# Performance work log

Hardware: AMD Instinct MI355X
Metric: run time of the kernel (lower is better)

Reference implementation:

```python
import jax, jax.numpy as jnp
import numpy as np

B, M = 1024, 200000
D_IN, DIM, D_OUT = 256, 128, 10
T = 1.0
EPS = 1e-7


def setup_inputs() -> dict:
    key = jax.random.key(0)
    k1, k2, k3, k4, k5 = jax.random.split(key, 5)
    x = jax.random.normal(k1, (B, D_IN), dtype=jnp.float32)
    y = jax.random.randint(k2, (B,), 0, D_OUT)
    candidate_x = jax.random.normal(k3, (M, D_IN), dtype=jnp.float32)
    candidate_y = jax.random.randint(k4, (M,), 0, D_OUT)
    W_enc = jax.random.normal(k5, (DIM, D_IN), dtype=jnp.float32) * (1.0 / np.sqrt(D_IN))
    b_enc = jnp.zeros((DIM,), dtype=jnp.float32)
    return {"x": x, "y": y, "candidate_x": candidate_x, "candidate_y": candidate_y,
            "W_enc": W_enc, "b_enc": b_enc, "is_train": 0}


def reference(x, y, candidate_x, candidate_y, W_enc, b_enc, is_train):
    # eval path (is_train == 0): no candidate subsampling, no diagonal masking
    h = x @ W_enc.T + b_enc            # [B, DIM]
    hc = candidate_x @ W_enc.T + b_enc  # [M, DIM]
    # pairwise L2 distance (cdist, p=2)
    sq = jnp.sum(h * h, axis=-1, keepdims=True) + jnp.sum(hc * hc, axis=-1)[None, :] \
         - 2.0 * (h @ hc.T)            # [B, M]
    dist = jnp.sqrt(jnp.maximum(sq, 0.0)) / T
    p = jax.nn.softmax(-dist, axis=-1)  # [B, M]
    y1h = jax.nn.one_hot(candidate_y, D_OUT, dtype=h.dtype)  # [M, D_OUT]
    logits = p @ y1h                    # [B, D_OUT]
    return jnp.log(logits + EPS)
```

## Files before the change

### kernel.cpp

```cpp
#include <hip/hip_runtime.h>
#include <hip/hip_bf16.h>
#include <math.h>

#define B_N   1024
#define M_N   200000
#define DIN   256
#define DIMN  128
#define DOUT  10
#define EPS_F 1e-7f
#define M_PAD 200064
#define NBY   1563
#define CTILES 8

typedef __bf16 bf16_t;
typedef __bf16 bf16x8 __attribute__((ext_vector_type(8)));
typedef float  f32x4  __attribute__((ext_vector_type(4)));


__global__ void cvt_w_kernel(const float* __restrict__ W, bf16_t* __restrict__ Wb){
    int i = blockIdx.x*256 + threadIdx.x;
    if (i < DIMN*DIN) Wb[i] = (bf16_t)W[i];
}

__global__ void hist_kernel(const int* __restrict__ cy, int* __restrict__ hist){
    __shared__ int h[DOUT];
    if (threadIdx.x < DOUT) h[threadIdx.x] = 0;
    __syncthreads();
    for (int i = blockIdx.x*blockDim.x + threadIdx.x; i < M_N; i += gridDim.x*blockDim.x)
        atomicAdd(&h[cy[i]], 1);
    __syncthreads();
    if (threadIdx.x < DOUT) atomicAdd(&hist[threadIdx.x*16], h[threadIdx.x]);
}

__global__ void prefix_kernel(const int* __restrict__ hist, int* __restrict__ cs){
    if (threadIdx.x == 0 && blockIdx.x == 0){
        int acc = 0;
        for (int c = 0; c < DOUT; ++c){ cs[c] = acc; acc += hist[c*16]; }
        cs[DOUT] = acc;
    }
}


__global__ __launch_bounds__(256) void encode_kernel(
    const float* __restrict__ src, const bf16_t* __restrict__ Wb,
    bf16_t* __restrict__ out, float* __restrict__ onorm, int N,
    const int* __restrict__ ycls, int* __restrict__ counters,
    const int* __restrict__ cs)
{
    __shared__ bf16_t As[128][136];
    __shared__ int   posL[128];
    __shared__ float nbuf[128][2];
    __shared__ int   cntL[DOUT], baseL[DOUT];
    const int tid = threadIdx.x;
    const int r0  = blockIdx.x*128;

    int myc = -1, myrank = 0;
    if (ycls != nullptr){
        if (tid < DOUT) cntL[tid] = 0;
        __syncthreads();
        if (tid < 128 && r0 + tid < N){
            myc = ycls[r0 + tid];
            myrank = atomicAdd(&cntL[myc], 1);
        }
        __syncthreads();
        if (tid < DOUT && cntL[tid] > 0)
            baseL[tid] = atomicAdd(&counters[tid*16], cntL[tid]);
        __syncthreads();
    }
    if (tid < 128)
        posL[tid] = (myc >= 0) ? (cs[myc] + baseL[myc] + myrank) : (r0 + tid);

    const int lane = tid & 63, wid = tid >> 6;
    const int wr = wid >> 1, wc = wid & 1;
    const int l15 = lane & 15, quad = lane >> 4;
    const int cbase = wc*64;

    f32x4 acc[4][4] = {};
    #pragma unroll
    for (int kh = 0; kh < 2; ++kh){
        __syncthreads();
        #pragma unroll
        for (int i = 0; i < 8; ++i){
            int idx = i*256 + tid;
            int row = idx >> 4;
            int col = (idx & 15)*8;
            int rr  = r0 + row; if (rr > N-1) rr = N-1;
            const float4* p4 = (const float4*)(src + (size_t)rr*DIN + kh*128 + col);
            float4 f0 = p4[0], f1 = p4[1];
            bf16x8 v;
            v[0]=(bf16_t)f0.x; v[1]=(bf16_t)f0.y; v[2]=(bf16_t)f0.z; v[3]=(bf16_t)f0.w;
            v[4]=(bf16_t)f1.x; v[5]=(bf16_t)f1.y; v[6]=(bf16_t)f1.z; v[7]=(bf16_t)f1.w;
            *(bf16x8*)&As[row][col] = v;
        }
        __syncthreads();
        #pragma unroll
        for (int ks = 0; ks < 4; ++ks){
            const int k  = ks*32 + quad*8;
            const int kg = kh*128 + k;
            bf16x8 a[4], b[4];
            #pragma unroll
            for (int rt = 0; rt < 4; ++rt)
                a[rt] = *(const bf16x8*)&As[wr*64 + rt*16 + l15][k];
            #pragma unroll
            for (int ct = 0; ct < 4; ++ct)
                b[ct] = *(const bf16x8*)(Wb + (size_t)(cbase + ct*16 + l15)*DIN + kg);
            #pragma unroll
            for (int rt = 0; rt < 4; ++rt)
                #pragma unroll
                for (int ct = 0; ct < 4; ++ct)
                    acc[rt][ct] = __builtin_amdgcn_mfma_f32_16x16x32_bf16(a[rt], b[ct], acc[rt][ct], 0, 0, 0);
        }
    }

    float np[4][4];
    #pragma unroll
    for (int rt = 0; rt < 4; ++rt)
        #pragma unroll
        for (int r = 0; r < 4; ++r){
            float s = 0.f;
            #pragma unroll
            for (int ct = 0; ct < 4; ++ct){ float v = acc[rt][ct][r]; s += v*v; }
            np[rt][r] = s;
        }
    #pragma unroll
    for (int m = 1; m < 16; m <<= 1)
        #pragma unroll
        for (int rt = 0; rt < 4; ++rt)
            #pragma unroll
            for (int r = 0; r < 4; ++r)
                np[rt][r] += __shfl_xor(np[rt][r], m, 64);
    if (l15 == 0){
        #pragma unroll
        for (int rt = 0; rt < 4; ++rt)
            #pragma unroll
            for (int r = 0; r < 4; ++r)
                nbuf[wr*64 + rt*16 + quad*4 + r][wc] = np[rt][r];
    }

    #pragma unroll
    for (int rt = 0; rt < 4; ++rt){
        #pragma unroll
        for (int r = 0; r < 4; ++r){
            int rl = wr*64 + rt*16 + quad*4 + r;
            if (r0 + rl < N){
                size_t rowp = (size_t)posL[rl]*DIMN;
                #pragma unroll
                for (int ct = 0; ct < 4; ++ct)
                    out[rowp + cbase + ct*16 + l15] = (bf16_t)acc[rt][ct][r];
            }
        }
    }
    __syncthreads();
    if (tid < 128){
        int rs = r0 + tid;
        if (rs < N) onorm[posL[tid]] = nbuf[tid][0] + nbuf[tid][1];
    }
}


__device__ __forceinline__ void bfly16(float (&s)[4][4]){
    #pragma unroll
    for (int m = 1; m < 16; m <<= 1)
        #pragma unroll
        for (int rt = 0; rt < 4; ++rt)
            #pragma unroll
            for (int r = 0; r < 4; ++r)
                s[rt][r] += __shfl_xor(s[rt][r], m, 64);
}

__device__ __forceinline__ void flushC(float (&s)[4][4], int c, int rbase,
                                       int quad, int l15, float* __restrict__ accG){
    bfly16(s);
    if (l15 == 0){
        #pragma unroll
        for (int rt = 0; rt < 4; ++rt)
            #pragma unroll
            for (int r = 0; r < 4; ++r)
                atomicAdd(&accG[(size_t)(rbase + rt*16 + quad*4 + r)*16 + c], s[rt][r]);
    }
}

__global__ __launch_bounds__(256, 2) void fused_kernel(
    const bf16_t* __restrict__ hb, const bf16_t* __restrict__ hcb,
    const float* __restrict__ hn, const float* __restrict__ hcn,
    const int* __restrict__ csg, float* __restrict__ accG)
{
    __shared__ bf16_t Bs[128][136];
    const int tid = threadIdx.x;
    const int lane = tid & 63, wid = tid >> 6;
    const int wr = wid >> 1, wc = wid & 1;
    const int l15 = lane & 15, quad = lane >> 4;
    const int rbase = blockIdx.x*128 + wr*64;

    bf16x8 a[4][4];
    #pragma unroll
    for (int ks = 0; ks < 4; ++ks)
        #pragma unroll
        for (int rt = 0; rt < 4; ++rt)
            a[ks][rt] = *(const bf16x8*)(hb + (size_t)(rbase + rt*16 + l15)*DIMN + ks*32 + quad*8);

    float hnv[4][4];
    #pragma unroll
    for (int rt = 0; rt < 4; ++rt)
        #pragma unroll
        for (int r = 0; r < 4; ++r)
            hnv[rt][r] = hn[rbase + rt*16 + quad*4 + r];

    int cseg[DOUT+1];
    #pragma unroll
    for (int i = 0; i <= DOUT; ++i) cseg[i] = csg[i];

    float s[4][4] = {};
    int curC = -1;

    for (int t = 0; t < CTILES; ++t){
        const int by = blockIdx.y*CTILES + t;
        if (by >= NBY) break;
        const int cbase0 = by*128;

        __syncthreads();
        #pragma unroll
        for (int i = 0; i < 8; ++i){
            int idx = i*256 + tid;
            int c   = idx >> 4;
            int k   = (idx & 15)*8;
            int cc  = cbase0 + c; if (cc > M_N-1) cc = M_N-1;
            *(bf16x8*)&Bs[c][k] = *(const bf16x8*)(hcb + (size_t)cc*DIMN + k);
        }
        __syncthreads();

        f32x4 acc[4][4] = {};
        #pragma unroll
        for (int ks = 0; ks < 4; ++ks){
            const int k = ks*32 + quad*8;
            bf16x8 b[4];
            #pragma unroll
            for (int ct = 0; ct < 4; ++ct)
                b[ct] = *(const bf16x8*)&Bs[wc*64 + ct*16 + l15][k];
            #pragma unroll
            for (int rt = 0; rt < 4; ++rt)
                #pragma unroll
                for (int ct = 0; ct < 4; ++ct)
                    acc[rt][ct] = __builtin_amdgcn_mfma_f32_16x16x32_bf16(a[ks][rt], b[ct], acc[rt][ct], 0, 0, 0);
        }

        float hcnv[4];
        #pragma unroll
        for (int ct = 0; ct < 4; ++ct){
            int cc = cbase0 + wc*64 + ct*16 + l15;
            hcnv[ct] = (cc < M_N) ? hcn[cc] : 1e30f;
        }
        #pragma unroll
        for (int rt = 0; rt < 4; ++rt)
            #pragma unroll
            for (int ct = 0; ct < 4; ++ct)
                #pragma unroll
                for (int r = 0; r < 4; ++r){
                    float sq = fmaxf(hnv[rt][r] + hcnv[ct] - 2.0f*acc[rt][ct][r], 0.0f);
                    acc[rt][ct][r] = __expf(-__builtin_amdgcn_sqrtf(sq));
                }

        const int lastc = min(cbase0 + 127, M_N - 1);
        int cLo = 0, cHi = 0;
        #pragma unroll
        for (int c = 1; c < DOUT; ++c){
            if (cbase0 >= cseg[c]) cLo = c;
            if (lastc  >= cseg[c]) cHi = c;
        }

        if (cLo == curC && cHi == curC){
            #pragma unroll
            for (int rt = 0; rt < 4; ++rt)
                #pragma unroll
                for (int r = 0; r < 4; ++r){
                    float v = 0.f;
                    #pragma unroll
                    for (int ct = 0; ct < 4; ++ct) v += acc[rt][ct][r];
                    s[rt][r] += v;
                }
        } else {
            if (curC >= 0) flushC(s, curC, rbase, quad, l15, accG);
            #pragma unroll
            for (int rt = 0; rt < 4; ++rt)
                #pragma unroll
                for (int r = 0; r < 4; ++r) s[rt][r] = 0.f;
            for (int c = cLo; c <= cHi; ++c){
                const int s0 = cseg[c], s1 = cseg[c+1];
                float m[4][4];
                #pragma unroll
                for (int rt = 0; rt < 4; ++rt)
                    #pragma unroll
                    for (int r = 0; r < 4; ++r){
                        float v = 0.f;
                        #pragma unroll
                        for (int ct = 0; ct < 4; ++ct){
                            int cc = cbase0 + wc*64 + ct*16 + l15;
                            v += (cc >= s0 && cc < s1) ? acc[rt][ct][r] : 0.f;
                        }
                        m[rt][r] = v;
                    }
                if (c == cHi){
                    #pragma unroll
                    for (int rt = 0; rt < 4; ++rt)
                        #pragma unroll
                        for (int r = 0; r < 4; ++r) s[rt][r] = m[rt][r];
                    curC = cHi;
                } else {
                    flushC(m, c, rbase, quad, l15, accG);
                }
            }
        }
    }
    if (curC >= 0) flushC(s, curC, rbase, quad, l15, accG);
}

__global__ void finalize_kernel(const float* __restrict__ accG, float* __restrict__ out){
    int b = blockIdx.x*blockDim.x + threadIdx.x;
    if (b < B_N){
        float v[DOUT]; float den = 0.f;
        #pragma unroll
        for (int c = 0; c < DOUT; ++c){ v[c] = accG[b*16 + c]; den += v[c]; }
        float inv = (den > 0.f) ? 1.0f/den : 0.f;
        #pragma unroll
        for (int c = 0; c < DOUT; ++c) out[b*DOUT + c] = logf(v[c]*inv + EPS_F);
    }
}


extern "C" void kernel_launch(void* const* d_in, const int* in_sizes, int n_in,
                              void* d_out, int out_size, void* d_ws, size_t ws_size,
                              hipStream_t stream)
{
    const float* x  = (const float*)d_in[0];
    const float* cx = (const float*)d_in[2];
    const int*   cy = (const int*)d_in[3];
    const float* W  = (const float*)d_in[4];
    float* out = (float*)d_out;

    char* w = (char*)d_ws;
    size_t off = 0;
    bf16_t* hcb = (bf16_t*)(w + off); off += (size_t)M_PAD*DIMN*2;
    bf16_t* hb  = (bf16_t*)(w + off); off += (size_t)B_N*DIMN*2;
    float*  hcn = (float*) (w + off); off += (size_t)M_PAD*4;
    float*  hn  = (float*) (w + off); off += (size_t)B_N*4;
    bf16_t* Wb  = (bf16_t*)(w + off); off += (size_t)DIMN*DIN*2;
    size_t zoff = off;
    float* accG = (float*)(w + off); off += (size_t)B_N*16*4;
    int* hist     = (int*)(w + off); off += 16*DOUT*4;
    int* counters = (int*)(w + off); off += 16*DOUT*4;
    int* csg      = (int*)(w + off); off += 64;
    size_t zsize = off - zoff;

    hipMemsetAsync(w + zoff, 0, zsize, stream);
    cvt_w_kernel<<<dim3((DIMN*DIN + 255)/256), dim3(256), 0, stream>>>(W, Wb);
    hist_kernel<<<dim3(256), dim3(256), 0, stream>>>(cy, hist);
    prefix_kernel<<<dim3(1), dim3(1), 0, stream>>>(hist, csg);
    encode_kernel<<<dim3(M_PAD/128), dim3(256), 0, stream>>>(cx, Wb, hcb, hcn, M_N, cy, counters, csg);
    encode_kernel<<<dim3(B_N/128), dim3(256), 0, stream>>>(x, Wb, hb, hn, B_N, nullptr, nullptr, nullptr);
    fused_kernel<<<dim3(B_N/128, (NBY + CTILES - 1)/CTILES), dim3(256), 0, stream>>>(hb, hcb, hn, hcn, csg, accG);
    finalize_kernel<<<dim3((B_N + 255)/256), dim3(256), 0, stream>>>(accG, out);
}
```

Measured before the change: 476.9 us.

## Double-buffer candidate tiles via direct global-to-LDS loads with XOR swizzle, 512 threads

Restructures the fused distance/softmax kernel so candidate tiles are staged into two LDS buffers with global_load_lds while the previous tile is computed. The LDS layout is XOR-swizzled to avoid bank conflicts, replacing the padded array. The block grows to 512 threads, with each wave handling 32 rows instead of 64, which cuts register use and raises occupancy. The cost is more atomics per row group in flush, plus added complexity and barrier ordering that must be right for the asynchronous LDS writes.

```diff
diff --git a/kernel.cpp b/kernel.cpp
--- a/kernel.cpp
+++ b/kernel.cpp
@@ -158,87 +158,98 @@
 }
 
 
-__device__ __forceinline__ void bfly16(float (&s)[4][4]){
+__device__ __forceinline__ void gld_lds16(const bf16_t* g, bf16_t* l){
+    __builtin_amdgcn_global_load_lds((const __attribute__((address_space(1))) void*)g,
+                                     (__attribute__((address_space(3))) void*)l, 16, 0, 0);
+}
+
+__device__ __forceinline__ void bfly16(float (&s)[2][4]){
     #pragma unroll
     for (int m = 1; m < 16; m <<= 1)
         #pragma unroll
-        for (int rt = 0; rt < 4; ++rt)
+        for (int rt = 0; rt < 2; ++rt)
             #pragma unroll
             for (int r = 0; r < 4; ++r)
                 s[rt][r] += __shfl_xor(s[rt][r], m, 64);
 }
 
-__device__ __forceinline__ void flushC(float (&s)[4][4], int c, int rbase,
+__device__ __forceinline__ void flushC(float (&s)[2][4], int c, int rbase,
                                        int quad, int l15, float* __restrict__ accG){
     bfly16(s);
     if (l15 == 0){
         #pragma unroll
-        for (int rt = 0; rt < 4; ++rt)
+        for (int rt = 0; rt < 2; ++rt)
             #pragma unroll
             for (int r = 0; r < 4; ++r)
                 atomicAdd(&accG[(size_t)(rbase + rt*16 + quad*4 + r)*16 + c], s[rt][r]);
     }
 }
 
-__global__ __launch_bounds__(256, 2) void fused_kernel(
+__global__ __launch_bounds__(512, 4) void fused_kernel(
     const bf16_t* __restrict__ hb, const bf16_t* __restrict__ hcb,
     const float* __restrict__ hn, const float* __restrict__ hcn,
     const int* __restrict__ csg, float* __restrict__ accG)
 {
-    __shared__ bf16_t Bs[128][136];
+    __shared__ bf16_t Bs0[128][128];
+    __shared__ bf16_t Bs1[128][128];
     const int tid = threadIdx.x;
     const int lane = tid & 63, wid = tid >> 6;
     const int wr = wid >> 1, wc = wid & 1;
     const int l15 = lane & 15, quad = lane >> 4;
-    const int rbase = blockIdx.x*128 + wr*64;
-
-    bf16x8 a[4][4];
+    const int rbase = blockIdx.x*128 + wr*32;
+
+    bf16x8 a[4][2];
     #pragma unroll
     for (int ks = 0; ks < 4; ++ks)
         #pragma unroll
-        for (int rt = 0; rt < 4; ++rt)
+        for (int rt = 0; rt < 2; ++rt)
             a[ks][rt] = *(const bf16x8*)(hb + (size_t)(rbase + rt*16 + l15)*DIMN + ks*32 + quad*8);
 
-    float hnv[4][4];
-    #pragma unroll
-    for (int rt = 0; rt < 4; ++rt)
+    float hnv[2][4];
+    #pragma unroll
+    for (int rt = 0; rt < 2; ++rt)
         #pragma unroll
         for (int r = 0; r < 4; ++r)
             hnv[rt][r] = hn[rbase + rt*16 + quad*4 + r];
 
     int cseg[DOUT+1];
     #pragma unroll
-    for (int i = 0; i <= DOUT; ++i) cseg[i] = csg[i];
-
-    float s[4][4] = {};
+    for (int i = 0; i <= DOUT; ++i) cseg[i] = __builtin_amdgcn_readfirstlane(csg[i]);
+
+    const int by0 = blockIdx.y*CTILES;
+    int nt = NBY - by0; if (nt > CTILES) nt = CTILES;
+
+    float s[2][4] = {};
     int curC = -1;
 
-    for (int t = 0; t < CTILES; ++t){
-        const int by = blockIdx.y*CTILES + t;
-        if (by >= NBY) break;
+    auto stage = [&](bf16_t (&Bsb)[128][128], int by){
+        const int cb = by*128;
+        #pragma unroll
+        for (int i = 0; i < 4; ++i){
+            int c   = i*512 + tid;
+            int col = c >> 4, j = c & 15;
+            int cc  = cb + col; if (cc > M_N-1) cc = M_N-1;
+            const bf16_t* g = hcb + (size_t)cc*DIMN + ((j ^ (col & 7)) << 3);
+            bf16_t* l = &Bsb[0][0] + ((i*512 + (wid << 6)) << 3);
+            gld_lds16(g, l);
+        }
+    };
+
+    auto compute = [&](const bf16_t (&Bsb)[128][128], int by){
         const int cbase0 = by*128;
-
-        __syncthreads();
-        #pragma unroll
-        for (int i = 0; i < 8; ++i){
-            int idx = i*256 + tid;
-            int c   = idx >> 4;
-            int k   = (idx & 15)*8;
-            int cc  = cbase0 + c; if (cc > M_N-1) cc = M_N-1;
-            *(bf16x8*)&Bs[c][k] = *(const bf16x8*)(hcb + (size_t)cc*DIMN + k);
-        }
-        __syncthreads();
-
-        f32x4 acc[4][4] = {};
+        f32x4 acc[2][4] = {};
+        const char* bsb = (const char*)&Bsb[0][0];
         #pragma unroll
         for (int ks = 0; ks < 4; ++ks){
-            const int k = ks*32 + quad*8;
             bf16x8 b[4];
             #pragma unroll
-            for (int ct = 0; ct < 4; ++ct)
-                b[ct] = *(const bf16x8*)&Bs[wc*64 + ct*16 + l15][k];
-            #pragma unroll
-            for (int rt = 0; rt < 4; ++rt)
+            for (int ct = 0; ct < 4; ++ct){
+                int row = wc*64 + ct*16 + l15;
+                int off = (row << 8) + ((((ks << 6) + (quad << 4))) ^ ((l15 & 7) << 4));
+                b[ct] = *(const bf16x8*)(bsb + off);
+            }
+            #pragma unroll
+            for (int rt = 0; rt < 2; ++rt)
                 #pragma unroll
                 for (int ct = 0; ct < 4; ++ct)
                     acc[rt][ct] = __builtin_amdgcn_mfma_f32_16x16x32_bf16(a[ks][rt], b[ct], acc[rt][ct], 0, 0, 0);
@@ -251,12 +262,12 @@
             hcnv[ct] = (cc < M_N) ? hcn[cc] : 1e30f;
         }
         #pragma unroll
-        for (int rt = 0; rt < 4; ++rt)
+        for (int rt = 0; rt < 2; ++rt)
             #pragma unroll
             for (int ct = 0; ct < 4; ++ct)
                 #pragma unroll
                 for (int r = 0; r < 4; ++r){
-                    float sq = fmaxf(hnv[rt][r] + hcnv[ct] - 2.0f*acc[rt][ct][r], 0.0f);
+                    float sq = fmaxf(fmaf(-2.0f, acc[rt][ct][r], hnv[rt][r] + hcnv[ct]), 0.0f);
                     acc[rt][ct][r] = __expf(-__builtin_amdgcn_sqrtf(sq));
                 }
 
@@ -270,25 +281,24 @@
 
         if (cLo == curC && cHi == curC){
             #pragma unroll
-            for (int rt = 0; rt < 4; ++rt)
+            for (int rt = 0; rt < 2; ++rt)
                 #pragma unroll
                 for (int r = 0; r < 4; ++r){
-                    float v = 0.f;
-                    #pragma unroll
-                    for (int ct = 0; ct < 4; ++ct) v += acc[rt][ct][r];
-                    s[rt][r] += v;
+                    float v0 = acc[rt][0][r] + acc[rt][1][r];
+                    float v1 = acc[rt][2][r] + acc[rt][3][r];
+                    s[rt][r] += v0 + v1;
                 }
         } else {
             if (curC >= 0) flushC(s, curC, rbase, quad, l15, accG);
             #pragma unroll
-            for (int rt = 0; rt < 4; ++rt)
+            for (int rt = 0; rt < 2; ++rt)
                 #pragma unroll
                 for (int r = 0; r < 4; ++r) s[rt][r] = 0.f;
             for (int c = cLo; c <= cHi; ++c){
                 const int s0 = cseg[c], s1 = cseg[c+1];
-                float m[4][4];
-                #pragma unroll
-                for (int rt = 0; rt < 4; ++rt)
+                float m[2][4];
+                #pragma unroll
+                for (int rt = 0; rt < 2; ++rt)
                     #pragma unroll
                     for (int r = 0; r < 4; ++r){
                         float v = 0.f;
@@ -301,7 +311,7 @@
                     }
                 if (c == cHi){
                     #pragma unroll
-                    for (int rt = 0; rt < 4; ++rt)
+                    for (int rt = 0; rt < 2; ++rt)
                         #pragma unroll
                         for (int r = 0; r < 4; ++r) s[rt][r] = m[rt][r];
                     curC = cHi;
@@ -310,6 +320,23 @@
                 }
             }
         }
+    };
+
+    stage(Bs0, by0);
+    __syncthreads();
+
+    #pragma unroll 1
+    for (int tp = 0; tp < CTILES/2; ++tp){
+        int t0 = tp*2;
+        if (t0 >= nt) break;
+        if (t0 + 1 < nt) stage(Bs1, by0 + t0 + 1);
+        compute(Bs0, by0 + t0);
+        __syncthreads();
+        int t1 = t0 + 1;
+        if (t1 >= nt) break;
+        if (t1 + 1 < nt) stage(Bs0, by0 + t1 + 1);
+        compute(Bs1, by0 + t1);
+        __syncthreads();
     }
     if (curC >= 0) flushC(s, curC, rbase, quad, l15, accG);
 }
@@ -357,6 +384,6 @@
     prefix_kernel<<<dim3(1), dim3(1), 0, stream>>>(hist, csg);
     encode_kernel<<<dim3(M_PAD/128), dim3(256), 0, stream>>>(cx, Wb, hcb, hcn, M_N, cy, counters, csg);
     encode_kernel<<<dim3(B_N/128), dim3(256), 0, stream>>>(x, Wb, hb, hn, B_N, nullptr, nullptr, nullptr);
-    fused_kernel<<<dim3(B_N/128, (NBY + CTILES - 1)/CTILES), dim3(256), 0, stream>>>(hb, hcb, hn, hcn, csg, accG);
+    fused_kernel<<<dim3(B_N/128, (NBY + CTILES - 1)/CTILES), dim3(512), 0, stream>>>(hb, hcb, hn, hcn, csg, accG);
     finalize_kernel<<<dim3((B_N + 255)/256), dim3(256), 0, stream>>>(accG, out);
 }
```

Measured after the change: 535.3 us. +12.2%, slower.
